# Kernel optimization log

Measured on AMD Instinct MI355X. Metric: run time of the kernel, lower is better.

Reference implementation:

```python
import jax, jax.numpy as jnp
import numpy as np

WIN = 8
HEADS = 4
DHEAD = 32
HID = HEADS * DHEAD  # 128


def setup_inputs() -> dict:
    key = jax.random.key(0)
    k1, k2, k3, k4 = jax.random.split(key, 4)
    x = jax.random.normal(k1, (1, 64, 48, 48, 48), dtype=jnp.float32)
    w_qkv = jax.random.normal(k2, (3 * HID, 64), dtype=jnp.float32) * 0.05  # Conv3d 1x1, no bias
    w_out = jax.random.normal(k3, (64, HID), dtype=jnp.float32) * 0.05     # merge_heads Conv3d 1x1
    b_out = jax.random.normal(k4, (64,), dtype=jnp.float32) * 0.05
    return {"x": x, "w_qkv": w_qkv, "w_out": w_out, "b_out": b_out}


def reference(x, w_qkv, w_out, b_out):
    B, C, H, W, D = x.shape
    X, Y, Z = H // WIN, W // WIN, D // WIN
    # 1x1x1 conv == channel matmul
    qkv = jnp.einsum('bcxyz,oc->boxyz', x, w_qkv)  # [B, 3*h*c, H, W, D]
    t = qkv.reshape(B, 3, HEADS, DHEAD, X, WIN, Y, WIN, Z, WIN)
    # -> [3, B, X, Y, Z, h, wx, wy, wz, c]
    t = t.transpose(1, 0, 4, 6, 8, 2, 5, 7, 9, 3)
    t = t.reshape(3, B * X * Y * Z, HEADS, WIN ** 3, DHEAD)
    q, k, v = t[0], t[1], t[2]
    scale = 1.0 / jnp.sqrt(jnp.asarray(DHEAD, dtype=q.dtype))
    scores = jnp.einsum('whnc,whmc->whnm', q, k) * scale  # [windows, h, 512, 512]
    attn = jax.nn.softmax(scores, axis=-1)
    out = jnp.einsum('whnm,whmc->whnc', attn, v)
    # merge windows back: -> [B, h*c, H, W, D]
    out = out.reshape(B, X, Y, Z, HEADS, WIN, WIN, WIN, DHEAD)
    out = out.transpose(0, 4, 8, 1, 5, 2, 6, 3, 7).reshape(B, HID, H, W, D)
    return jnp.einsum('bcxyz,oc->boxyz', out, w_out) + b_out[None, :, None, None, None]
```

## Files before the change

kernel.cpp:

```cpp
#include <hip/hip_runtime.h>
#include <hip/hip_bf16.h>
#include <stdint.h>

#define NWIN 216
#define NVOX 110592

typedef __bf16 bf16_t;
typedef __attribute__((ext_vector_type(8))) __bf16 bf16x8;
typedef __attribute__((ext_vector_type(4))) __bf16 bf16x4;
typedef __attribute__((ext_vector_type(4))) float f32x4;
typedef __attribute__((ext_vector_type(16))) float f32x16;
typedef __attribute__((ext_vector_type(4))) unsigned int u32x4;
typedef __attribute__((ext_vector_type(2))) unsigned int u32x2;

__device__ __forceinline__ f32x4 mfma16(bf16x8 a, bf16x8 b, f32x4 c) {
  return __builtin_amdgcn_mfma_f32_16x16x32_bf16(a, b, c, 0, 0, 0);
}
__device__ __forceinline__ f32x16 mfma32(bf16x8 a, bf16x8 b, f32x16 c) {
  return __builtin_amdgcn_mfma_f32_32x32x16_bf16(a, b, c, 0, 0, 0);
}

__device__ __forceinline__ float fexp2(float x) {
  return __builtin_amdgcn_exp2f(x);
}

__device__ __forceinline__ unsigned int pk2(float lo, float hi) {
  unsigned short l = __builtin_bit_cast(unsigned short, (bf16_t)lo);
  unsigned short h = __builtin_bit_cast(unsigned short, (bf16_t)hi);
  return (unsigned int)l | ((unsigned int)h << 16);
}

__device__ __forceinline__ void swap_half(unsigned int& a, unsigned int& b) {
#if __has_builtin(__builtin_amdgcn_permlane32_swap)
  u32x2 r = __builtin_amdgcn_permlane32_swap(a, b, false, false);
  a = r[0]; b = r[1];
#else
  asm("v_permlane32_swap_b32 %0, %1" : "+v"(a), "+v"(b));
#endif
}

__global__ __launch_bounds__(512, 2) void qkv_kernel(const float* __restrict__ x,
                                                     const float* __restrict__ w_qkv,
                                                     bf16_t* __restrict__ qkv) {
  __shared__ bf16_t xs[512][72];
  const int w = blockIdx.x;
  const int wx = w / 36, wy = (w / 6) % 6, wz = w % 6;
  const int t = threadIdx.x;
  const int lane = t & 63;
  const int q16 = lane & 15, g = lane >> 4;
  const float SC = 0.25505003946337226f;

  #pragma unroll
  for (int i = 0; i < 4; ++i) {
    int seg = t + 512 * i;
    int cpair = seg & 31, xy = seg >> 5;
    int ix = xy >> 3, iy = xy & 7;
    const float* s0 = x + (((2 * cpair) * 48 + wx * 8 + ix) * 48 + wy * 8 + iy) * 48 + wz * 8;
    const float* s1 = s0 + 48 * 48 * 48;
    float4 a0 = reinterpret_cast<const float4*>(s0)[0];
    float4 a1 = reinterpret_cast<const float4*>(s0)[1];
    float4 b0 = reinterpret_cast<const float4*>(s1)[0];
    float4 b1 = reinterpret_cast<const float4*>(s1)[1];
    float av[8] = {a0.x, a0.y, a0.z, a0.w, a1.x, a1.y, a1.z, a1.w};
    float bv[8] = {b0.x, b0.y, b0.z, b0.w, b1.x, b1.y, b1.z, b1.w};
    #pragma unroll
    for (int z = 0; z < 8; ++z)
      *(unsigned int*)&xs[xy * 8 + z][2 * cpair] = pk2(av[z], bv[z]);
  }

  const int wv = t >> 6;
  bf16x8 aw[3][2];
  #pragma unroll
  for (int j = 0; j < 3; ++j) {
    int o = wv * 48 + j * 16 + q16;
    float sc = (o < 128) ? SC : 1.0f;
    #pragma unroll
    for (int s = 0; s < 2; ++s) {
      const float* wr = w_qkv + o * 64 + s * 32 + 8 * g;
      float4 u0 = reinterpret_cast<const float4*>(wr)[0];
      float4 u1 = reinterpret_cast<const float4*>(wr)[1];
      bf16x8 f;
      f[0]=(bf16_t)(u0.x*sc); f[1]=(bf16_t)(u0.y*sc); f[2]=(bf16_t)(u0.z*sc); f[3]=(bf16_t)(u0.w*sc);
      f[4]=(bf16_t)(u1.x*sc); f[5]=(bf16_t)(u1.y*sc); f[6]=(bf16_t)(u1.z*sc); f[7]=(bf16_t)(u1.w*sc);
      aw[j][s] = f;
    }
  }
  __syncthreads();

  for (int nt = 0; nt < 32; ++nt) {
    int n = nt * 16 + q16;
    bf16x8 xb0 = *(const bf16x8*)&xs[n][8 * g];
    bf16x8 xb1 = *(const bf16x8*)&xs[n][32 + 8 * g];
    #pragma unroll
    for (int j = 0; j < 3; ++j) {
      f32x4 acc = {0.f, 0.f, 0.f, 0.f};
      acc = mfma16(aw[j][0], xb0, acc);
      acc = mfma16(aw[j][1], xb1, acc);
      int ob = wv * 48 + j * 16 + 4 * g;
      int sel = ob >> 7, rem = ob & 127, hh = rem >> 5, dd = rem & 31;
      bf16x4 pk;
      pk[0] = (bf16_t)acc[0]; pk[1] = (bf16_t)acc[1];
      pk[2] = (bf16_t)acc[2]; pk[3] = (bf16_t)acc[3];
      *(bf16x4*)(qkv + ((((size_t)sel * NWIN + w) * 4 + hh) * 512 + n) * 32 + dd) = pk;
    }
  }
}


__device__ __forceinline__ void attn_step(bf16x8 kf0, bf16x8 kf1, bf16x8 vf0, bf16x8 vf1,
                                          bf16x8 q0, bf16x8 q1, const f32x16& z, bf16x8 ones,
                                          f32x16& O, f32x16& Sm) {
  f32x16 S = mfma32(kf0, q0, z);
  S = mfma32(kf1, q1, S);
  #pragma unroll
  for (int r = 0; r < 16; ++r) S[r] = fexp2(S[r]);
  unsigned int p01 = pk2(S[0], S[1]),   p23 = pk2(S[2], S[3]);
  unsigned int p45 = pk2(S[4], S[5]),   p67 = pk2(S[6], S[7]);
  unsigned int p89 = pk2(S[8], S[9]),   pab = pk2(S[10], S[11]);
  unsigned int pcd = pk2(S[12], S[13]), pef = pk2(S[14], S[15]);
  swap_half(p01, p45);
  swap_half(p23, p67);
  swap_half(p89, pcd);
  swap_half(pab, pef);
  u32x4 u0 = {p01, p23, p45, p67};
  u32x4 u1 = {p89, pab, pcd, pef};
  bf16x8 pf0 = __builtin_bit_cast(bf16x8, u0);
  bf16x8 pf1 = __builtin_bit_cast(bf16x8, u1);
  O = mfma32(pf0, vf0, O);
  O = mfma32(pf1, vf1, O);
  Sm = mfma32(pf0, ones, Sm);
  Sm = mfma32(pf1, ones, Sm);
}

__global__ __launch_bounds__(512, 2) void attn_kernel(const bf16_t* __restrict__ qkv,
                                                      bf16_t* __restrict__ att) {
  __shared__ bf16_t vt[32][520];
  const int blk = blockIdx.x;
  const int wh = blk >> 1, half = blk & 1;
  const int w = wh >> 2, h = wh & 3;
  const bf16_t* qb = qkv + ((size_t)(0 * NWIN + w) * 4 + h) * 16384;
  const bf16_t* kb = qkv + ((size_t)(1 * NWIN + w) * 4 + h) * 16384;
  const bf16_t* vb = qkv + ((size_t)(2 * NWIN + w) * 4 + h) * 16384;
  const int t = threadIdx.x, lane = t & 63, wv = t >> 6;
  const int l31 = lane & 31, hi = lane >> 5;
  const int qbase = half * 256 + wv * 32;

  bf16x8 qf0 = *(const bf16x8*)(qb + (qbase + l31) * 32 + 8 * hi);
  bf16x8 qf1 = *(const bf16x8*)(qb + (qbase + l31) * 32 + 16 + 8 * hi);

  #pragma unroll
  for (int i = 0; i < 2; ++i) {
    int task = i * 512 + t;
    int p = task >> 2, dg = task & 3;
    bf16x8 v0 = *(const bf16x8*)(vb + (2 * p) * 32 + 8 * dg);
    bf16x8 v1 = *(const bf16x8*)(vb + (2 * p + 1) * 32 + 8 * dg);
    u32x4 a = __builtin_bit_cast(u32x4, v0);
    u32x4 b = __builtin_bit_cast(u32x4, v1);
    #pragma unroll
    for (int j = 0; j < 4; ++j) {
      unsigned int lo = (a[j] & 0xffffu) | (b[j] << 16);
      unsigned int hh = (a[j] >> 16) | (b[j] & 0xffff0000u);
      *(unsigned int*)&vt[dg * 8 + 2 * j][2 * p]     = lo;
      *(unsigned int*)&vt[dg * 8 + 2 * j + 1][2 * p] = hh;
    }
  }
  __syncthreads();

  f32x16 O = {}, Sm = {};
  const f32x16 z = {};
  bf16x8 ones;
  #pragma unroll
  for (int e = 0; e < 8; ++e) ones[e] = (bf16_t)1.0f;

  const bf16_t* kptr = kb + l31 * 32 + 8 * hi;
  bf16x8 kf0 = *(const bf16x8*)(kptr);
  bf16x8 kf1 = *(const bf16x8*)(kptr + 16);
  for (int kt = 0; kt < 15; ++kt) {
    const bf16_t* nk = kptr + (kt + 1) * 1024;
    bf16x8 nkf0 = *(const bf16x8*)(nk);
    bf16x8 nkf1 = *(const bf16x8*)(nk + 16);
    bf16x8 vf0 = *(const bf16x8*)&vt[l31][kt * 32 + 8 * hi];
    bf16x8 vf1 = *(const bf16x8*)&vt[l31][kt * 32 + 8 * hi + 16];
    attn_step(kf0, kf1, vf0, vf1, qf0, qf1, z, ones, O, Sm);
    kf0 = nkf0; kf1 = nkf1;
  }
  {
    bf16x8 vf0 = *(const bf16x8*)&vt[l31][15 * 32 + 8 * hi];
    bf16x8 vf1 = *(const bf16x8*)&vt[l31][15 * 32 + 8 * hi + 16];
    attn_step(kf0, kf1, vf0, vf1, qf0, qf1, z, ones, O, Sm);
  }

  #pragma unroll
  for (int r = 0; r < 16; ++r) {
    int qr = (r & 3) + 8 * (r >> 2) + 4 * hi;
    int n = qbase + qr;
    float ri = __builtin_amdgcn_rcpf(Sm[r]);
    att[((size_t)w * 512 + n) * 128 + h * 32 + l31] = (bf16_t)(O[r] * ri);
  }
}

__global__ __launch_bounds__(256) void proj_kernel(const bf16_t* __restrict__ att,
                                                   const float* __restrict__ w_out,
                                                   const float* __restrict__ b_out,
                                                   float* __restrict__ out) {
  __shared__ bf16_t ws[64][136];
  const int blk = blockIdx.x;
  const int w = blk >> 2, quarter = blk & 3;
  const int wx = w / 36, wy = (w / 6) % 6, wz = w % 6;
  const int t = threadIdx.x, lane = t & 63, wv = t >> 6;
  const int q16 = lane & 15, g = lane >> 4;

  {
    int o = t >> 2, c0 = (t & 3) * 32;
    const float* wr = w_out + o * 128 + c0;
    #pragma unroll
    for (int u = 0; u < 4; ++u) {
      float4 a = reinterpret_cast<const float4*>(wr)[2 * u];
      float4 b = reinterpret_cast<const float4*>(wr)[2 * u + 1];
      *(unsigned int*)&ws[o][c0 + 8 * u]     = pk2(a.x, a.y);
      *(unsigned int*)&ws[o][c0 + 8 * u + 2] = pk2(a.z, a.w);
      *(unsigned int*)&ws[o][c0 + 8 * u + 4] = pk2(b.x, b.y);
      *(unsigned int*)&ws[o][c0 + 8 * u + 6] = pk2(b.z, b.w);
    }
  }
  float4 bias[4];
  #pragma unroll
  for (int ot = 0; ot < 4; ++ot)
    bias[ot] = *reinterpret_cast<const float4*>(b_out + ot * 16 + 4 * g);
  __syncthreads();

  bf16x8 aw[4][4];
  #pragma unroll
  for (int ot = 0; ot < 4; ++ot)
    #pragma unroll
    for (int kc = 0; kc < 4; ++kc)
      aw[ot][kc] = *(const bf16x8*)&ws[ot * 16 + q16][kc * 32 + 8 * g];

  #pragma unroll
  for (int i = 0; i < 2; ++i) {
    int n = quarter * 128 + (wv * 2 + i) * 16 + q16;
    const bf16_t* ar = att + ((size_t)w * 512 + n) * 128;
    bf16x8 bf[4];
    #pragma unroll
    for (int kc = 0; kc < 4; ++kc)
      bf[kc] = *(const bf16x8*)(ar + kc * 32 + 8 * g);
    int ix = n >> 6, iy = (n >> 3) & 7, iz = n & 7;
    int v = ((wx * 8 + ix) * 48 + wy * 8 + iy) * 48 + wz * 8 + iz;
    #pragma unroll
    for (int ot = 0; ot < 4; ++ot) {
      f32x4 acc = {0.f, 0.f, 0.f, 0.f};
      #pragma unroll
      for (int kc = 0; kc < 4; ++kc)
        acc = mfma16(aw[ot][kc], bf[kc], acc);
      #pragma unroll
      for (int r = 0; r < 4; ++r) {
        int o = ot * 16 + 4 * g + r;
        out[(size_t)o * NVOX + v] = acc[r] + ((const float*)&bias[ot])[r];
      }
    }
  }
}

extern "C" void kernel_launch(void* const* d_in, const int* in_sizes, int n_in,
                              void* d_out, int out_size, void* d_ws, size_t ws_size,
                              hipStream_t stream) {
  const float* x     = (const float*)d_in[0];
  const float* w_qkv = (const float*)d_in[1];
  const float* w_out = (const float*)d_in[2];
  const float* b_out = (const float*)d_in[3];
  float* out = (float*)d_out;
  bf16_t* qkv = (bf16_t*)d_ws;
  bf16_t* att = (bf16_t*)((char*)d_ws + (size_t)3 * NWIN * 4 * 512 * 32 * 2);
  qkv_kernel<<<dim3(NWIN), dim3(512), 0, stream>>>(x, w_qkv, qkv);
  attn_kernel<<<dim3(NWIN * 4 * 2), dim3(512), 0, stream>>>(qkv, att);
  proj_kernel<<<dim3(NWIN * 4), dim3(256), 0, stream>>>(att, w_out, b_out, out);
}
```

Baseline: 108.7 us.

## Fuse QKV projection into attention kernel, keeping K/V fragments in LDS

Merges the separate QKV projection kernel into the attention kernel. Each block now loads its window's input voxels, computes Q for its own rows and K/V for all 512 keys directly into MFMA fragment layout in shared memory, then runs the attention loop from LDS. This removes the qkv workspace round trip through global memory and one kernel launch. In exchange, the input window load and K/V projection are repeated 8 times per window (4 heads x 2 halves), and the larger LDS footprint lowers occupancy to one block per CU.

```diff
diff --git a/kernel.cpp b/kernel.cpp
--- a/kernel.cpp
+++ b/kernel.cpp
@@ -7,7 +7,6 @@
 
 typedef __bf16 bf16_t;
 typedef __attribute__((ext_vector_type(8))) __bf16 bf16x8;
-typedef __attribute__((ext_vector_type(4))) __bf16 bf16x4;
 typedef __attribute__((ext_vector_type(4))) float f32x4;
 typedef __attribute__((ext_vector_type(16))) float f32x16;
 typedef __attribute__((ext_vector_type(4))) unsigned int u32x4;
@@ -39,15 +38,49 @@
 #endif
 }
 
-__global__ __launch_bounds__(512, 2) void qkv_kernel(const float* __restrict__ x,
-                                                     const float* __restrict__ w_qkv,
-                                                     bf16_t* __restrict__ qkv) {
+__device__ __forceinline__ void pack_fr(const f32x16& S, bf16x8& f0, bf16x8& f1) {
+  unsigned int p01 = pk2(S[0], S[1]),   p23 = pk2(S[2], S[3]);
+  unsigned int p45 = pk2(S[4], S[5]),   p67 = pk2(S[6], S[7]);
+  unsigned int p89 = pk2(S[8], S[9]),   pab = pk2(S[10], S[11]);
+  unsigned int pcd = pk2(S[12], S[13]), pef = pk2(S[14], S[15]);
+  swap_half(p01, p45);
+  swap_half(p23, p67);
+  swap_half(p89, pcd);
+  swap_half(pab, pef);
+  u32x4 u0 = {p01, p23, p45, p67};
+  u32x4 u1 = {p89, pab, pcd, pef};
+  f0 = __builtin_bit_cast(bf16x8, u0);
+  f1 = __builtin_bit_cast(bf16x8, u1);
+}
+
+
+__device__ __forceinline__ void attn_step(bf16x8 kf0, bf16x8 kf1, bf16x8 vf0, bf16x8 vf1,
+                                          bf16x8 q0, bf16x8 q1, const f32x16& z, bf16x8 ones,
+                                          f32x16& O, f32x16& Sm) {
+  f32x16 S = mfma32(kf0, q0, z);
+  S = mfma32(kf1, q1, S);
+  #pragma unroll
+  for (int r = 0; r < 16; ++r) S[r] = fexp2(S[r]);
+  bf16x8 pf0, pf1;
+  pack_fr(S, pf0, pf1);
+  O = mfma32(pf0, vf0, O);
+  O = mfma32(pf1, vf1, O);
+  Sm = mfma32(pf0, ones, Sm);
+  Sm = mfma32(pf1, ones, Sm);
+}
+
+__global__ __launch_bounds__(512, 1) void fattn_kernel(const float* __restrict__ x,
+                                                       const float* __restrict__ w_qkv,
+                                                       bf16_t* __restrict__ att) {
   __shared__ bf16_t xs[512][72];
-  const int w = blockIdx.x;
+  __shared__ u32x4 kfl[16][2][64];
+  __shared__ u32x4 vfl[16][2][64];
+  const int blk = blockIdx.x;
+  const int wh = blk >> 1, half = blk & 1;
+  const int w = wh >> 2, h = wh & 3;
   const int wx = w / 36, wy = (w / 6) % 6, wz = w % 6;
-  const int t = threadIdx.x;
-  const int lane = t & 63;
-  const int q16 = lane & 15, g = lane >> 4;
+  const int t = threadIdx.x, lane = t & 63, wv = t >> 6;
+  const int l31 = lane & 31, hi = lane >> 5;
   const float SC = 0.25505003946337226f;
 
   #pragma unroll
@@ -64,129 +97,78 @@
     float av[8] = {a0.x, a0.y, a0.z, a0.w, a1.x, a1.y, a1.z, a1.w};
     float bv[8] = {b0.x, b0.y, b0.z, b0.w, b1.x, b1.y, b1.z, b1.w};
     #pragma unroll
-    for (int z = 0; z < 8; ++z)
-      *(unsigned int*)&xs[xy * 8 + z][2 * cpair] = pk2(av[z], bv[z]);
-  }
-
-  const int wv = t >> 6;
-  bf16x8 aw[3][2];
-  #pragma unroll
-  for (int j = 0; j < 3; ++j) {
-    int o = wv * 48 + j * 16 + q16;
-    float sc = (o < 128) ? SC : 1.0f;
-    #pragma unroll
-    for (int s = 0; s < 2; ++s) {
-      const float* wr = w_qkv + o * 64 + s * 32 + 8 * g;
-      float4 u0 = reinterpret_cast<const float4*>(wr)[0];
-      float4 u1 = reinterpret_cast<const float4*>(wr)[1];
-      bf16x8 f;
-      f[0]=(bf16_t)(u0.x*sc); f[1]=(bf16_t)(u0.y*sc); f[2]=(bf16_t)(u0.z*sc); f[3]=(bf16_t)(u0.w*sc);
-      f[4]=(bf16_t)(u1.x*sc); f[5]=(bf16_t)(u1.y*sc); f[6]=(bf16_t)(u1.z*sc); f[7]=(bf16_t)(u1.w*sc);
-      aw[j][s] = f;
+    for (int z8 = 0; z8 < 8; ++z8)
+      *(unsigned int*)&xs[xy * 8 + z8][2 * cpair] = pk2(av[z8], bv[z8]);
+  }
+
+  bf16x8 wqf[4], wkf[4], wvf[4];
+  #pragma unroll
+  for (int cch = 0; cch < 4; ++cch) {
+    const float* q_r = w_qkv + (h * 32 + l31) * 64 + cch * 16 + 8 * hi;
+    const float* k_r = q_r + 128 * 64;
+    const float* v_r = q_r + 256 * 64;
+    float4 u0, u1;
+    bf16x8 f;
+    u0 = reinterpret_cast<const float4*>(q_r)[0]; u1 = reinterpret_cast<const float4*>(q_r)[1];
+    f[0]=(bf16_t)(u0.x*SC); f[1]=(bf16_t)(u0.y*SC); f[2]=(bf16_t)(u0.z*SC); f[3]=(bf16_t)(u0.w*SC);
+    f[4]=(bf16_t)(u1.x*SC); f[5]=(bf16_t)(u1.y*SC); f[6]=(bf16_t)(u1.z*SC); f[7]=(bf16_t)(u1.w*SC);
+    wqf[cch] = f;
+    u0 = reinterpret_cast<const float4*>(k_r)[0]; u1 = reinterpret_cast<const float4*>(k_r)[1];
+    f[0]=(bf16_t)u0.x; f[1]=(bf16_t)u0.y; f[2]=(bf16_t)u0.z; f[3]=(bf16_t)u0.w;
+    f[4]=(bf16_t)u1.x; f[5]=(bf16_t)u1.y; f[6]=(bf16_t)u1.z; f[7]=(bf16_t)u1.w;
+    wkf[cch] = f;
+    u0 = reinterpret_cast<const float4*>(v_r)[0]; u1 = reinterpret_cast<const float4*>(v_r)[1];
+    f[0]=(bf16_t)u0.x; f[1]=(bf16_t)u0.y; f[2]=(bf16_t)u0.z; f[3]=(bf16_t)u0.w;
+    f[4]=(bf16_t)u1.x; f[5]=(bf16_t)u1.y; f[6]=(bf16_t)u1.z; f[7]=(bf16_t)u1.w;
+    wvf[cch] = f;
+  }
+  __syncthreads();
+
+  const f32x16 z = {};
+  const int qbase = half * 256 + wv * 32;
+
+  f32x16 Dq = z;
+  #pragma unroll
+  for (int cch = 0; cch < 4; ++cch) {
+    bf16x8 xb = *(const bf16x8*)&xs[qbase + l31][cch * 16 + 8 * hi];
+    Dq = mfma32(wqf[cch], xb, Dq);
+  }
+  bf16x8 qf0, qf1;
+  pack_fr(Dq, qf0, qf1);
+
+  #pragma unroll
+  for (int i = 0; i < 2; ++i) {
+    int kt = 2 * wv + i;
+    bf16x8 xf[4];
+    #pragma unroll
+    for (int cch = 0; cch < 4; ++cch)
+      xf[cch] = *(const bf16x8*)&xs[kt * 32 + l31][cch * 16 + 8 * hi];
+    f32x16 Dk = z, Dv = z;
+    #pragma unroll
+    for (int cch = 0; cch < 4; ++cch) {
+      Dk = mfma32(wkf[cch], xf[cch], Dk);
+      Dv = mfma32(xf[cch], wvf[cch], Dv);
     }
+    bf16x8 a, b;
+    pack_fr(Dk, a, b);
+    kfl[kt][0][lane] = __builtin_bit_cast(u32x4, a);
+    kfl[kt][1][lane] = __builtin_bit_cast(u32x4, b);
+    pack_fr(Dv, a, b);
+    vfl[kt][0][lane] = __builtin_bit_cast(u32x4, a);
+    vfl[kt][1][lane] = __builtin_bit_cast(u32x4, b);
   }
   __syncthreads();
 
-  for (int nt = 0; nt < 32; ++nt) {
-    int n = nt * 16 + q16;
-    bf16x8 xb0 = *(const bf16x8*)&xs[n][8 * g];
-    bf16x8 xb1 = *(const bf16x8*)&xs[n][32 + 8 * g];
-    #pragma unroll
-    for (int j = 0; j < 3; ++j) {
-      f32x4 acc = {0.f, 0.f, 0.f, 0.f};
-      acc = mfma16(aw[j][0], xb0, acc);
-      acc = mfma16(aw[j][1], xb1, acc);
-      int ob = wv * 48 + j * 16 + 4 * g;
-      int sel = ob >> 7, rem = ob & 127, hh = rem >> 5, dd = rem & 31;
-      bf16x4 pk;
-      pk[0] = (bf16_t)acc[0]; pk[1] = (bf16_t)acc[1];
-      pk[2] = (bf16_t)acc[2]; pk[3] = (bf16_t)acc[3];
-      *(bf16x4*)(qkv + ((((size_t)sel * NWIN + w) * 4 + hh) * 512 + n) * 32 + dd) = pk;
-    }
-  }
-}
-
-
-__device__ __forceinline__ void attn_step(bf16x8 kf0, bf16x8 kf1, bf16x8 vf0, bf16x8 vf1,
-                                          bf16x8 q0, bf16x8 q1, const f32x16& z, bf16x8 ones,
-                                          f32x16& O, f32x16& Sm) {
-  f32x16 S = mfma32(kf0, q0, z);
-  S = mfma32(kf1, q1, S);
-  #pragma unroll
-  for (int r = 0; r < 16; ++r) S[r] = fexp2(S[r]);
-  unsigned int p01 = pk2(S[0], S[1]),   p23 = pk2(S[2], S[3]);
-  unsigned int p45 = pk2(S[4], S[5]),   p67 = pk2(S[6], S[7]);
-  unsigned int p89 = pk2(S[8], S[9]),   pab = pk2(S[10], S[11]);
-  unsigned int pcd = pk2(S[12], S[13]), pef = pk2(S[14], S[15]);
-  swap_half(p01, p45);
-  swap_half(p23, p67);
-  swap_half(p89, pcd);
-  swap_half(pab, pef);
-  u32x4 u0 = {p01, p23, p45, p67};
-  u32x4 u1 = {p89, pab, pcd, pef};
-  bf16x8 pf0 = __builtin_bit_cast(bf16x8, u0);
-  bf16x8 pf1 = __builtin_bit_cast(bf16x8, u1);
-  O = mfma32(pf0, vf0, O);
-  O = mfma32(pf1, vf1, O);
-  Sm = mfma32(pf0, ones, Sm);
-  Sm = mfma32(pf1, ones, Sm);
-}
-
-__global__ __launch_bounds__(512, 2) void attn_kernel(const bf16_t* __restrict__ qkv,
-                                                      bf16_t* __restrict__ att) {
-  __shared__ bf16_t vt[32][520];
-  const int blk = blockIdx.x;
-  const int wh = blk >> 1, half = blk & 1;
-  const int w = wh >> 2, h = wh & 3;
-  const bf16_t* qb = qkv + ((size_t)(0 * NWIN + w) * 4 + h) * 16384;
-  const bf16_t* kb = qkv + ((size_t)(1 * NWIN + w) * 4 + h) * 16384;
-  const bf16_t* vb = qkv + ((size_t)(2 * NWIN + w) * 4 + h) * 16384;
-  const int t = threadIdx.x, lane = t & 63, wv = t >> 6;
-  const int l31 = lane & 31, hi = lane >> 5;
-  const int qbase = half * 256 + wv * 32;
-
-  bf16x8 qf0 = *(const bf16x8*)(qb + (qbase + l31) * 32 + 8 * hi);
-  bf16x8 qf1 = *(const bf16x8*)(qb + (qbase + l31) * 32 + 16 + 8 * hi);
-
-  #pragma unroll
-  for (int i = 0; i < 2; ++i) {
-    int task = i * 512 + t;
-    int p = task >> 2, dg = task & 3;
-    bf16x8 v0 = *(const bf16x8*)(vb + (2 * p) * 32 + 8 * dg);
-    bf16x8 v1 = *(const bf16x8*)(vb + (2 * p + 1) * 32 + 8 * dg);
-    u32x4 a = __builtin_bit_cast(u32x4, v0);
-    u32x4 b = __builtin_bit_cast(u32x4, v1);
-    #pragma unroll
-    for (int j = 0; j < 4; ++j) {
-      unsigned int lo = (a[j] & 0xffffu) | (b[j] << 16);
-      unsigned int hh = (a[j] >> 16) | (b[j] & 0xffff0000u);
-      *(unsigned int*)&vt[dg * 8 + 2 * j][2 * p]     = lo;
-      *(unsigned int*)&vt[dg * 8 + 2 * j + 1][2 * p] = hh;
-    }
-  }
-  __syncthreads();
-
   f32x16 O = {}, Sm = {};
-  const f32x16 z = {};
   bf16x8 ones;
   #pragma unroll
   for (int e = 0; e < 8; ++e) ones[e] = (bf16_t)1.0f;
 
-  const bf16_t* kptr = kb + l31 * 32 + 8 * hi;
-  bf16x8 kf0 = *(const bf16x8*)(kptr);
-  bf16x8 kf1 = *(const bf16x8*)(kptr + 16);
-  for (int kt = 0; kt < 15; ++kt) {
-    const bf16_t* nk = kptr + (kt + 1) * 1024;
-    bf16x8 nkf0 = *(const bf16x8*)(nk);
-    bf16x8 nkf1 = *(const bf16x8*)(nk + 16);
-    bf16x8 vf0 = *(const bf16x8*)&vt[l31][kt * 32 + 8 * hi];
-    bf16x8 vf1 = *(const bf16x8*)&vt[l31][kt * 32 + 8 * hi + 16];
-    attn_step(kf0, kf1, vf0, vf1, qf0, qf1, z, ones, O, Sm);
-    kf0 = nkf0; kf1 = nkf1;
-  }
-  {
-    bf16x8 vf0 = *(const bf16x8*)&vt[l31][15 * 32 + 8 * hi];
-    bf16x8 vf1 = *(const bf16x8*)&vt[l31][15 * 32 + 8 * hi + 16];
+  for (int kt = 0; kt < 16; ++kt) {
+    bf16x8 kf0 = __builtin_bit_cast(bf16x8, kfl[kt][0][lane]);
+    bf16x8 kf1 = __builtin_bit_cast(bf16x8, kfl[kt][1][lane]);
+    bf16x8 vf0 = __builtin_bit_cast(bf16x8, vfl[kt][0][lane]);
+    bf16x8 vf1 = __builtin_bit_cast(bf16x8, vfl[kt][1][lane]);
     attn_step(kf0, kf1, vf0, vf1, qf0, qf1, z, ones, O, Sm);
   }
 
@@ -269,9 +251,7 @@
   const float* w_out = (const float*)d_in[2];
   const float* b_out = (const float*)d_in[3];
   float* out = (float*)d_out;
-  bf16_t* qkv = (bf16_t*)d_ws;
-  bf16_t* att = (bf16_t*)((char*)d_ws + (size_t)3 * NWIN * 4 * 512 * 32 * 2);
-  qkv_kernel<<<dim3(NWIN), dim3(512), 0, stream>>>(x, w_qkv, qkv);
-  attn_kernel<<<dim3(NWIN * 4 * 2), dim3(512), 0, stream>>>(qkv, att);
+  bf16_t* att = (bf16_t*)d_ws;
+  fattn_kernel<<<dim3(NWIN * 4 * 2), dim3(512), 0, stream>>>(x, w_qkv, att);
   proj_kernel<<<dim3(NWIN * 4), dim3(256), 0, stream>>>(att, w_out, b_out, out);
 }
```

Result: slower. 165.6 us (+52.4%).
